# Performance work log

Measured on AMD Instinct MI355X. Metric: run time of the kernel, lower is better.

## Reference

```python
import jax, jax.numpy as jnp
import numpy as np

B, C_IN, H, W = 8, 128, 64, 64
C_KEY, C_VAL, C_OUT = 64, 64, 128
BN_EPS = 1e-5
NORM_EPS = 1e-7


def setup_inputs() -> dict:
    key = jax.random.key(0)
    ks = jax.random.split(key, 8)
    s = 0.02
    return {
        "query_feature": jax.random.normal(ks[0], (B, C_IN, H, W), jnp.float32),
        "key_feature": jax.random.normal(ks[1], (B, C_IN, H, W), jnp.float32),
        "value_feature": jax.random.normal(ks[2], (B, C_IN, H, W), jnp.float32),
        "Wk": jax.random.normal(ks[3], (C_KEY, C_IN), jnp.float32) * s,  # shared f_key/f_query 1x1 conv
        "bk": jnp.zeros((C_KEY,), jnp.float32),
        "gamma": jnp.ones((C_KEY,), jnp.float32),   # BatchNorm2d weight
        "beta": jnp.zeros((C_KEY,), jnp.float32),   # BatchNorm2d bias
        "Wv": jax.random.normal(ks[4], (C_VAL, C_IN), jnp.float32) * s,
        "bv": jnp.zeros((C_VAL,), jnp.float32),
        "Ww": jax.random.normal(ks[5], (C_OUT, C_VAL), jnp.float32) * s,  # zero-init in original; random for nontrivial output
        "bw": jnp.zeros((C_OUT,), jnp.float32),
    }


def _conv1x1(x, w, b):
    # x: [B,C,H,W], w: [O,C] -> [B,O,H,W]
    return jnp.einsum('bchw,oc->bohw', x, w) + b[None, :, None, None]


def _bn_train(y, gamma, beta):
    # BatchNorm2d in train mode: batch stats over (B,H,W) per channel
    m = y.mean(axis=(0, 2, 3), keepdims=True)
    v = y.var(axis=(0, 2, 3), keepdims=True)
    return (y - m) * jax.lax.rsqrt(v + BN_EPS) * gamma[None, :, None, None] + beta[None, :, None, None]


def reference(query_feature, key_feature, value_feature, Wk, bk, gamma, beta, Wv, bv, Ww, bw):
    b, _, h, w = query_feature.shape
    n = h * w

    def f_key(x):
        return _bn_train(_conv1x1(x, Wk, bk), gamma, beta)

    # query: [B,N,Ck], key: [B,Ck,N], value: [B,N,Cv]
    q = f_key(query_feature).reshape(b, C_KEY, n).transpose(0, 2, 1)
    k = f_key(key_feature).reshape(b, C_KEY, n)
    v = _conv1x1(value_feature, Wv, bv).reshape(b, C_VAL, n).transpose(0, 2, 1)

    # L2-normalize over channel dim (cosine similarity)
    q = q / (jnp.linalg.norm(q, axis=2, keepdims=True) + NORM_EPS)
    k = k / (jnp.linalg.norm(k, axis=1, keepdims=True) + NORM_EPS)

    sim = jnp.einsum('bnc,bcm->bnm', q, k) + 1.0     # [B,N,N], no softmax
    ctx = jnp.einsum('bnm,bmv->bnv', sim, v)         # [B,N,Cv]
    ctx = ctx.transpose(0, 2, 1).reshape(b, C_VAL, h, w)
    return _conv1x1(ctx, Ww, bw)
```

## Files before the change

kernel.cpp:

```cpp
#include <hip/hip_runtime.h>
#include <math.h>

#define NTOT 4096
#define NBATCH 8
#define CIN 128
#define CK 64
#define CV 64
#define CO 128
#define BN_COUNT 32768.0f

#define OFF_YQ    0ul
#define OFF_YK    2097152ul
#define OFF_V     4194304ul
#define OFF_STATS 6291456ul
#define OFF_VSUM  6307840ul
#define OFF_MP    2097152ul
#define OFF_DP    2228224ul

__global__ __launch_bounds__(256) void gemm3_fused(
    const float* __restrict__ Xq, const float* __restrict__ Xk, const float* __restrict__ Xv,
    const float* __restrict__ Wk, const float* __restrict__ bk,
    const float* __restrict__ Wv, const float* __restrict__ bv,
    float* __restrict__ Yq, float* __restrict__ Yk, float* __restrict__ Vv,
    float* __restrict__ stats, float* __restrict__ vsum)
{
    const int chunk = blockIdx.x;
    const int b     = blockIdx.y;
    const int which = blockIdx.z;
    const float* X    = (which == 0) ? Xq : (which == 1) ? Xk : Xv;
    const float* W    = (which == 2) ? Wv : Wk;
    const float* bias = (which == 2) ? bv : bk;
    float* Y          = (which == 0) ? Yq : (which == 1) ? Yk : Vv;

    __shared__ float sX[CIN][128];

    const int t = threadIdx.x;
    const int lane = t & 63;
    const int wu = __builtin_amdgcn_readfirstlane(t >> 6);

    const int n0 = chunk * 128;
    const float* Xb = X + (size_t)b * (CIN * NTOT) + n0;

#pragma unroll
    for (int r = 0; r < 16; ++r) {
        int idx4 = t + r * 256;
        int c  = idx4 >> 5;
        int j4 = (idx4 & 31) << 2;
        float4 xv = *(const float4*)(Xb + (size_t)c * NTOT + j4);
        *(float4*)&sX[c][j4] = xv;
    }
    __syncthreads();

    const float* Wp = W + (size_t)wu * 16 * CIN;
    float a0[16], a1[16];
#pragma unroll
    for (int ki = 0; ki < 16; ++ki) { a0[ki] = 0.f; a1[ki] = 0.f; }

#pragma unroll 8
    for (int c = 0; c < CIN; ++c) {
        float x0 = sX[c][lane];
        float x1 = sX[c][lane + 64];
#pragma unroll
        for (int ki = 0; ki < 16; ++ki) {
            float w = Wp[ki * CIN + c];
            a0[ki] += x0 * w;
            a1[ki] += x1 * w;
        }
    }

    float* Yb = Y + (size_t)b * (CK * NTOT) + n0;
#pragma unroll
    for (int ki = 0; ki < 16; ++ki) {
        const int o = wu * 16 + ki;
        const float bo = bias[o];
        float y0 = a0[ki] + bo;
        float y1 = a1[ki] + bo;
        Yb[(size_t)o * NTOT + lane]      = y0;
        Yb[(size_t)o * NTOT + lane + 64] = y1;
        a0[ki] = y0 + y1;
        a1[ki] = y0 * y0 + y1 * y1;
    }

#pragma unroll
    for (int off = 32; off > 0; off >>= 1) {
#pragma unroll
        for (int ki = 0; ki < 16; ++ki) {
            a0[ki] += __shfl_down(a0[ki], off, 64);
            a1[ki] += __shfl_down(a1[ki], off, 64);
        }
    }
    if (lane == 0) {
        if (which < 2) {
            float* sb = stats + (size_t)(b * 2 + which) * 1024;
#pragma unroll
            for (int ki = 0; ki < 16; ++ki) {
                const int o = wu * 16 + ki;
                atomicAdd(&sb[o * 16],     a0[ki]);
                atomicAdd(&sb[o * 16 + 4], a1[ki]);
            }
        } else {
            float* vb = vsum + (size_t)b * 1024;
#pragma unroll
            for (int ki = 0; ki < 16; ++ki)
                atomicAdd(&vb[(wu * 16 + ki) * 16], a0[ki]);
        }
    }
}

__global__ __launch_bounds__(256) void kv_kernel(
    const float* __restrict__ Yk, const float* __restrict__ Vv,
    const float* __restrict__ stats, const float* __restrict__ gamma,
    const float* __restrict__ beta, float* __restrict__ KVp)
{
    const int chunk = blockIdx.x;
    const int b     = blockIdx.y;
    __shared__ float sk[64][68];
    __shared__ float sv[64][68];
    __shared__ float rn[64];
    __shared__ float sscl[64], sshf[64];

    const int t = threadIdx.x;
    if (t < 64) {
        float S = 0.f, SS = 0.f;
#pragma unroll
        for (int bb = 0; bb < 8; ++bb) {
            const float* sb = stats + (size_t)(bb * 2 + 1) * 1024 + t * 16;
            S  += sb[0];
            SS += sb[4];
        }
        float mean = S * (1.f / BN_COUNT);
        float var  = SS * (1.f / BN_COUNT) - mean * mean;
        float scl  = gamma[t] * rsqrtf(var + 1e-5f);
        sscl[t] = scl;
        sshf[t] = beta[t] - mean * scl;
    }
    __syncthreads();

    const int n0 = chunk * 64;
    const float* Ykb = Yk + (size_t)b * (CK * NTOT) + n0;
    const float* Vb  = Vv + (size_t)b * (CK * NTOT) + n0;

#pragma unroll
    for (int r = 0; r < 4; ++r) {
        int idx4 = t + r * 256;
        int c  = idx4 >> 4;
        int j4 = (idx4 & 15) << 2;
        float4 kf = *(const float4*)(Ykb + (size_t)c * NTOT + j4);
        float4 vf = *(const float4*)(Vb  + (size_t)c * NTOT + j4);
        float scl = sscl[c], sh = sshf[c];
        float4 ks = make_float4(kf.x * scl + sh, kf.y * scl + sh,
                                kf.z * scl + sh, kf.w * scl + sh);
        *(float4*)&sk[c][j4] = ks;
        *(float4*)&sv[c][j4] = vf;
    }
    __syncthreads();

    if (t < 64) {
        float ssum = 0.f;
#pragma unroll 8
        for (int c = 0; c < 64; ++c) { float x = sk[c][t]; ssum += x * x; }
        rn[t] = 1.f / (sqrtf(ssum) + 1e-7f);
    }
    __syncthreads();
#pragma unroll
    for (int r = 0; r < 16; ++r) {
        int idx = t + r * 256;
        sk[idx >> 6][idx & 63] *= rn[idx & 63];
    }
    __syncthreads();

    const int tc = t >> 4, tv = t & 15;
    float acc[4][4];
#pragma unroll
    for (int i = 0; i < 4; ++i)
#pragma unroll
        for (int k2 = 0; k2 < 4; ++k2) acc[i][k2] = 0.f;

#pragma unroll 2
    for (int jq = 0; jq < 16; ++jq) {
        float4 a4[4], b4[4];
#pragma unroll
        for (int i = 0; i < 4; ++i)  a4[i] = *(const float4*)&sk[tc * 4 + i][jq * 4];
#pragma unroll
        for (int k2 = 0; k2 < 4; ++k2) b4[k2] = *(const float4*)&sv[tv * 4 + k2][jq * 4];
#pragma unroll
        for (int i = 0; i < 4; ++i)
#pragma unroll
            for (int k2 = 0; k2 < 4; ++k2) {
                acc[i][k2] += a4[i].x * b4[k2].x + a4[i].y * b4[k2].y
                            + a4[i].z * b4[k2].z + a4[i].w * b4[k2].w;
            }
    }

    float* P = KVp + ((size_t)(b * 64 + chunk)) * 4096;
#pragma unroll
    for (int i = 0; i < 4; ++i) {
        float4 st = make_float4(acc[i][0], acc[i][1], acc[i][2], acc[i][3]);
        *(float4*)&P[(tc * 4 + i) * 64 + tv * 4] = st;
    }
}

__global__ __launch_bounds__(256) void m_kernel(
    const float* __restrict__ KVp, const float* __restrict__ vsum,
    const float* __restrict__ Ww, const float* __restrict__ bw,
    float* __restrict__ Mp, float* __restrict__ dp)
{
    const int half = blockIdx.x;
    const int b    = blockIdx.y;
    __shared__ float sKV[64][36];
    __shared__ float sWw[128][36];
    __shared__ float svs[32];
    const int t = threadIdx.x;

#pragma unroll
    for (int r = 0; r < 4; ++r) {
        int idx4 = t + r * 256;
        int o  = idx4 >> 3;
        int v4 = (idx4 & 7) << 2;
        *(float4*)&sWw[o][v4] = *(const float4*)(Ww + (size_t)o * 64 + half * 32 + v4);
    }
    if (t < 32) svs[t] = vsum[((size_t)b * 64 + half * 32 + t) * 16];

    const float* base = KVp + (size_t)b * 64 * 4096;
    const int c0  = t >> 3;
    const int vq0 = (t & 7) << 2;
    const size_t off0 = (size_t)c0 * 64 + half * 32 + vq0;
    const size_t off1 = (size_t)(c0 + 32) * 64 + half * 32 + vq0;
    float4 r0 = make_float4(0.f, 0.f, 0.f, 0.f);
    float4 r1 = make_float4(0.f, 0.f, 0.f, 0.f);
#pragma unroll 4
    for (int ch = 0; ch < 64; ++ch) {
        const float* pc = base + (size_t)ch * 4096;
        float4 x0 = *(const float4*)(pc + off0);
        float4 x1 = *(const float4*)(pc + off1);
        r0.x += x0.x; r0.y += x0.y; r0.z += x0.z; r0.w += x0.w;
        r1.x += x1.x; r1.y += x1.y; r1.z += x1.z; r1.w += x1.w;
    }
    *(float4*)&sKV[c0][vq0]      = r0;
    *(float4*)&sKV[c0 + 32][vq0] = r1;
    __syncthreads();

    const int c  = t & 63;
    const int og = (t >> 6) * 32;
    float kreg[32];
#pragma unroll
    for (int vq = 0; vq < 8; ++vq) {
        float4 kv4 = *(const float4*)&sKV[c][vq * 4];
        kreg[vq * 4 + 0] = kv4.x; kreg[vq * 4 + 1] = kv4.y;
        kreg[vq * 4 + 2] = kv4.z; kreg[vq * 4 + 3] = kv4.w;
    }
    float* Mpb = Mp + ((size_t)b * 2 + half) * 8192;
#pragma unroll
    for (int oi = 0; oi < 32; ++oi) {
        const int o = og + oi;
        float acc = 0.f;
#pragma unroll
        for (int vq = 0; vq < 8; ++vq) {
            float4 w4 = *(const float4*)&sWw[o][vq * 4];
            acc += kreg[vq * 4 + 0] * w4.x + kreg[vq * 4 + 1] * w4.y
                 + kreg[vq * 4 + 2] * w4.z + kreg[vq * 4 + 3] * w4.w;
        }
        Mpb[(size_t)c * CO + o] = acc;
    }

    if (t < 128) {
        float acc = (half == 0) ? bw[t] : 0.f;
#pragma unroll 8
        for (int v = 0; v < 32; ++v) acc += sWw[t][v] * svs[v];
        dp[((size_t)b * 2 + half) * 128 + t] = acc;
    }
}

__global__ __launch_bounds__(256) void out_kernel(
    const float* __restrict__ Yq, const float* __restrict__ stats,
    const float* __restrict__ gamma, const float* __restrict__ beta,
    const float* __restrict__ Mp, const float* __restrict__ dp,
    float* __restrict__ out)
{
    const int chunk = blockIdx.x;
    const int b     = blockIdx.y;
    __shared__ float sM[CK * CO];
    __shared__ float sq[64][68];
    __shared__ float rn[64];
    __shared__ float sd[CO];
    __shared__ float sscl[64], sshf[64];

    const int t = threadIdx.x;
    const int n0 = chunk * 64;

    const float* Mp0 = Mp + (size_t)b * 2 * 8192;
    const float* Mp1 = Mp0 + 8192;
#pragma unroll
    for (int r = 0; r < 8; ++r) {
        int idx4 = t + r * 256;
        float4 m0 = ((const float4*)Mp0)[idx4];
        float4 m1 = ((const float4*)Mp1)[idx4];
        ((float4*)sM)[idx4] = make_float4(m0.x + m1.x, m0.y + m1.y,
                                          m0.z + m1.z, m0.w + m1.w);
    }
    if (t < CO) sd[t] = dp[(size_t)b * 2 * 128 + t] + dp[((size_t)b * 2 + 1) * 128 + t];
    if (t < 64) {
        float S = 0.f, SS = 0.f;
#pragma unroll
        for (int bb = 0; bb < 8; ++bb) {
            const float* sb = stats + (size_t)(bb * 2) * 1024 + t * 16;
            S  += sb[0];
            SS += sb[4];
        }
        float mean = S * (1.f / BN_COUNT);
        float var  = SS * (1.f / BN_COUNT) - mean * mean;
        float scl  = gamma[t] * rsqrtf(var + 1e-5f);
        sscl[t] = scl;
        sshf[t] = beta[t] - mean * scl;
    }
    __syncthreads();

    const float* Yb = Yq + (size_t)b * (CK * NTOT) + n0;
#pragma unroll
    for (int r = 0; r < 4; ++r) {
        int idx4 = t + r * 256;
        int c  = idx4 >> 4;
        int j4 = (idx4 & 15) << 2;
        float4 xv = *(const float4*)(Yb + (size_t)c * NTOT + j4);
        float scl = sscl[c], sh = sshf[c];
        sq[c][j4 + 0] = xv.x * scl + sh;
        sq[c][j4 + 1] = xv.y * scl + sh;
        sq[c][j4 + 2] = xv.z * scl + sh;
        sq[c][j4 + 3] = xv.w * scl + sh;
    }
    __syncthreads();
    if (t < 64) {
        float ssum = 0.f;
#pragma unroll 8
        for (int c = 0; c < 64; ++c) { float x = sq[c][t]; ssum += x * x; }
        rn[t] = 1.f / (sqrtf(ssum) + 1e-7f);
    }
    __syncthreads();

    const int j0 = (t & 15) << 2;
    const int o0 = (t >> 4) << 3;
    float acc[4][8];
#pragma unroll
    for (int jj = 0; jj < 4; ++jj)
#pragma unroll
        for (int oo = 0; oo < 8; ++oo) acc[jj][oo] = 0.f;

#pragma unroll 4
    for (int c = 0; c < 64; ++c) {
        float4 qv = *(const float4*)&sq[c][j0];
        float4 m0 = *(const float4*)&sM[c * CO + o0];
        float4 m1 = *(const float4*)&sM[c * CO + o0 + 4];
        float aq[4] = {qv.x, qv.y, qv.z, qv.w};
        float am[8] = {m0.x, m0.y, m0.z, m0.w, m1.x, m1.y, m1.z, m1.w};
#pragma unroll
        for (int jj = 0; jj < 4; ++jj)
#pragma unroll
            for (int oo = 0; oo < 8; ++oo) acc[jj][oo] += aq[jj] * am[oo];
    }

    float4 rq = *(const float4*)&rn[j0];
    float rnj[4] = {rq.x, rq.y, rq.z, rq.w};

    float* outb = out + (size_t)b * (CO * NTOT) + n0;
#pragma unroll
    for (int oo = 0; oo < 8; ++oo) {
        float dd = sd[o0 + oo];
        float4 st = make_float4(acc[0][oo] * rnj[0] + dd,
                                acc[1][oo] * rnj[1] + dd,
                                acc[2][oo] * rnj[2] + dd,
                                acc[3][oo] * rnj[3] + dd);
        *(float4*)&outb[(size_t)(o0 + oo) * NTOT + j0] = st;
    }
}

extern "C" void kernel_launch(void* const* d_in, const int* in_sizes, int n_in,
                              void* d_out, int out_size, void* d_ws, size_t ws_size,
                              hipStream_t stream) {
    (void)in_sizes; (void)n_in; (void)out_size; (void)ws_size;
    const float* q     = (const float*)d_in[0];
    const float* k     = (const float*)d_in[1];
    const float* v     = (const float*)d_in[2];
    const float* Wk    = (const float*)d_in[3];
    const float* bk    = (const float*)d_in[4];
    const float* gamma = (const float*)d_in[5];
    const float* beta  = (const float*)d_in[6];
    const float* Wv    = (const float*)d_in[7];
    const float* bv    = (const float*)d_in[8];
    const float* Ww    = (const float*)d_in[9];
    const float* bw    = (const float*)d_in[10];
    float* out = (float*)d_out;
    float* ws  = (float*)d_ws;

    float* Yq    = ws + OFF_YQ;
    float* Yk    = ws + OFF_YK;
    float* Vv    = ws + OFF_V;
    float* stats = ws + OFF_STATS;
    float* vsum  = ws + OFF_VSUM;
    float* Mp    = ws + OFF_MP;
    float* dp    = ws + OFF_DP;
    float* KVp   = out;

    hipMemsetAsync(stats, 0, (16384 + 8192) * sizeof(float), stream);

    gemm3_fused<<<dim3(32, NBATCH, 3), 256, 0, stream>>>(
        q, k, v, Wk, bk, Wv, bv, Yq, Yk, Vv, stats, vsum);
    kv_kernel<<<dim3(64, NBATCH), 256, 0, stream>>>(Yk, Vv, stats, gamma, beta, KVp);
    m_kernel<<<dim3(2, NBATCH), 256, 0, stream>>>(KVp, vsum, Ww, bw, Mp, dp);
    out_kernel<<<dim3(64, NBATCH), 256, 0, stream>>>(Yq, stats, gamma, beta, Mp, dp, out);
}
```

Baseline: 203.3 us.

## Split BN statistics into separate kernel and shrink projection GEMM tiles

The projection GEMM now computes 64 columns per block instead of 128, which doubles the grid to 1536 blocks and removes the in-kernel shuffle reductions and atomics for BN statistics. A new stats_kernel re-reads Yq and Yk to accumulate per-channel sums into a single global slot, and the value-sum reduction moves into kv_kernel. The L2-norm computation in kv and out kernels is spread across all four waves, and kv folds the normalization into the operand loads. The cost is an extra launch and an extra full read of Yq and Yk (about 16 MB).

```diff
diff --git a/kernel.cpp b/kernel.cpp
--- a/kernel.cpp
+++ b/kernel.cpp
@@ -13,16 +13,15 @@
 #define OFF_YK    2097152ul
 #define OFF_V     4194304ul
 #define OFF_STATS 6291456ul
-#define OFF_VSUM  6307840ul
+#define OFF_VSUM  6293504ul
 #define OFF_MP    2097152ul
 #define OFF_DP    2228224ul
 
-__global__ __launch_bounds__(256) void gemm3_fused(
+__global__ __launch_bounds__(256) void gemm3_kernel(
     const float* __restrict__ Xq, const float* __restrict__ Xk, const float* __restrict__ Xv,
     const float* __restrict__ Wk, const float* __restrict__ bk,
     const float* __restrict__ Wv, const float* __restrict__ bv,
-    float* __restrict__ Yq, float* __restrict__ Yk, float* __restrict__ Vv,
-    float* __restrict__ stats, float* __restrict__ vsum)
+    float* __restrict__ Yq, float* __restrict__ Yk, float* __restrict__ Vv)
 {
     const int chunk = blockIdx.x;
     const int b     = blockIdx.y;
@@ -32,102 +31,103 @@
     const float* bias = (which == 2) ? bv : bk;
     float* Y          = (which == 0) ? Yq : (which == 1) ? Yk : Vv;
 
-    __shared__ float sX[CIN][128];
+    __shared__ float sX[CIN][64];
 
     const int t = threadIdx.x;
     const int lane = t & 63;
     const int wu = __builtin_amdgcn_readfirstlane(t >> 6);
 
-    const int n0 = chunk * 128;
+    const int n0 = chunk * 64;
     const float* Xb = X + (size_t)b * (CIN * NTOT) + n0;
 
 #pragma unroll
-    for (int r = 0; r < 16; ++r) {
+    for (int r = 0; r < 8; ++r) {
         int idx4 = t + r * 256;
-        int c  = idx4 >> 5;
-        int j4 = (idx4 & 31) << 2;
+        int c  = idx4 >> 4;
+        int j4 = (idx4 & 15) << 2;
         float4 xv = *(const float4*)(Xb + (size_t)c * NTOT + j4);
         *(float4*)&sX[c][j4] = xv;
     }
     __syncthreads();
 
     const float* Wp = W + (size_t)wu * 16 * CIN;
-    float a0[16], a1[16];
-#pragma unroll
-    for (int ki = 0; ki < 16; ++ki) { a0[ki] = 0.f; a1[ki] = 0.f; }
+    float acc[16];
+#pragma unroll
+    for (int ki = 0; ki < 16; ++ki) acc[ki] = 0.f;
 
 #pragma unroll 8
     for (int c = 0; c < CIN; ++c) {
-        float x0 = sX[c][lane];
-        float x1 = sX[c][lane + 64];
-#pragma unroll
-        for (int ki = 0; ki < 16; ++ki) {
-            float w = Wp[ki * CIN + c];
-            a0[ki] += x0 * w;
-            a1[ki] += x1 * w;
-        }
+        float xv = sX[c][lane];
+#pragma unroll
+        for (int ki = 0; ki < 16; ++ki)
+            acc[ki] += xv * Wp[ki * CIN + c];
     }
 
     float* Yb = Y + (size_t)b * (CK * NTOT) + n0;
 #pragma unroll
     for (int ki = 0; ki < 16; ++ki) {
-        const int o = wu * 16 + ki;
-        const float bo = bias[o];
-        float y0 = a0[ki] + bo;
-        float y1 = a1[ki] + bo;
-        Yb[(size_t)o * NTOT + lane]      = y0;
-        Yb[(size_t)o * NTOT + lane + 64] = y1;
-        a0[ki] = y0 + y1;
-        a1[ki] = y0 * y0 + y1 * y1;
-    }
-
+        int o = wu * 16 + ki;
+        Yb[(size_t)o * NTOT + lane] = acc[ki] + bias[o];
+    }
+}
+
+__global__ __launch_bounds__(256) void stats_kernel(
+    const float* __restrict__ Yq, const float* __restrict__ Yk,
+    float* __restrict__ stats)
+{
+    const int nsplit = blockIdx.x;
+    const int c      = blockIdx.y;
+    const int which  = blockIdx.z;
+    const float* Y = which ? Yk : Yq;
+    const int t = threadIdx.x;
+
+    float s = 0.f, ss = 0.f;
+#pragma unroll
+    for (int p = 0; p < 4; ++p) {
+        int b = (t >> 7) + p * 2;
+        int e = (t & 127) << 2;
+        const float* src = Y + (size_t)b * (CK * NTOT) + (size_t)c * NTOT
+                         + nsplit * 512 + e;
+        float4 v = *(const float4*)src;
+        s  += v.x + v.y + v.z + v.w;
+        ss += v.x * v.x + v.y * v.y + v.z * v.z + v.w * v.w;
+    }
 #pragma unroll
     for (int off = 32; off > 0; off >>= 1) {
-#pragma unroll
-        for (int ki = 0; ki < 16; ++ki) {
-            a0[ki] += __shfl_down(a0[ki], off, 64);
-            a1[ki] += __shfl_down(a1[ki], off, 64);
-        }
-    }
-    if (lane == 0) {
-        if (which < 2) {
-            float* sb = stats + (size_t)(b * 2 + which) * 1024;
-#pragma unroll
-            for (int ki = 0; ki < 16; ++ki) {
-                const int o = wu * 16 + ki;
-                atomicAdd(&sb[o * 16],     a0[ki]);
-                atomicAdd(&sb[o * 16 + 4], a1[ki]);
-            }
-        } else {
-            float* vb = vsum + (size_t)b * 1024;
-#pragma unroll
-            for (int ki = 0; ki < 16; ++ki)
-                atomicAdd(&vb[(wu * 16 + ki) * 16], a0[ki]);
-        }
+        s  += __shfl_down(s, off, 64);
+        ss += __shfl_down(ss, off, 64);
+    }
+    __shared__ float red[8];
+    int wave = t >> 6, lane = t & 63;
+    if (lane == 0) { red[wave * 2] = s; red[wave * 2 + 1] = ss; }
+    __syncthreads();
+    if (t == 0) {
+        float S  = red[0] + red[2] + red[4] + red[6];
+        float SS = red[1] + red[3] + red[5] + red[7];
+        atomicAdd(&stats[(which * 64 + c) * 16],     S);
+        atomicAdd(&stats[(which * 64 + c) * 16 + 4], SS);
     }
 }
 
 __global__ __launch_bounds__(256) void kv_kernel(
     const float* __restrict__ Yk, const float* __restrict__ Vv,
     const float* __restrict__ stats, const float* __restrict__ gamma,
-    const float* __restrict__ beta, float* __restrict__ KVp)
+    const float* __restrict__ beta, float* __restrict__ KVp,
+    float* __restrict__ vsum)
 {
     const int chunk = blockIdx.x;
     const int b     = blockIdx.y;
     __shared__ float sk[64][68];
     __shared__ float sv[64][68];
+    __shared__ float pn[4][64];
     __shared__ float rn[64];
     __shared__ float sscl[64], sshf[64];
 
     const int t = threadIdx.x;
+    const int wave = t >> 6, lane = t & 63;
     if (t < 64) {
-        float S = 0.f, SS = 0.f;
-#pragma unroll
-        for (int bb = 0; bb < 8; ++bb) {
-            const float* sb = stats + (size_t)(bb * 2 + 1) * 1024 + t * 16;
-            S  += sb[0];
-            SS += sb[4];
-        }
+        float S  = stats[(64 + t) * 16];
+        float SS = stats[(64 + t) * 16 + 4];
         float mean = S * (1.f / BN_COUNT);
         float var  = SS * (1.f / BN_COUNT) - mean * mean;
         float scl  = gamma[t] * rsqrtf(var + 1e-5f);
@@ -155,18 +155,24 @@
     }
     __syncthreads();
 
-    if (t < 64) {
-        float ssum = 0.f;
-#pragma unroll 8
-        for (int c = 0; c < 64; ++c) { float x = sk[c][t]; ssum += x * x; }
-        rn[t] = 1.f / (sqrtf(ssum) + 1e-7f);
-    }
-    __syncthreads();
-#pragma unroll
-    for (int r = 0; r < 16; ++r) {
-        int idx = t + r * 256;
-        sk[idx >> 6][idx & 63] *= rn[idx & 63];
-    }
+    {
+        float s = 0.f;
+#pragma unroll
+        for (int i = 0; i < 16; ++i) { float x = sk[wave * 16 + i][lane]; s += x * x; }
+        pn[wave][lane] = s;
+    }
+    {
+        const int v = t >> 2, q = t & 3;
+        float s = 0.f;
+#pragma unroll
+        for (int i = 0; i < 16; ++i) s += sv[v][q * 16 + i];
+        s += __shfl_down(s, 2, 64);
+        s += __shfl_down(s, 1, 64);
+        if (q == 0) atomicAdd(&vsum[((size_t)b * 64 + v) * 16], s);
+    }
+    __syncthreads();
+    if (t < 64)
+        rn[t] = 1.f / (sqrtf(pn[0][t] + pn[1][t] + pn[2][t] + pn[3][t]) + 1e-7f);
     __syncthreads();
 
     const int tc = t >> 4, tv = t & 15;
@@ -178,9 +184,13 @@
 
 #pragma unroll 2
     for (int jq = 0; jq < 16; ++jq) {
+        float4 rq = *(const float4*)&rn[jq * 4];
         float4 a4[4], b4[4];
 #pragma unroll
-        for (int i = 0; i < 4; ++i)  a4[i] = *(const float4*)&sk[tc * 4 + i][jq * 4];
+        for (int i = 0; i < 4; ++i) {
+            float4 k4 = *(const float4*)&sk[tc * 4 + i][jq * 4];
+            a4[i] = make_float4(k4.x * rq.x, k4.y * rq.y, k4.z * rq.z, k4.w * rq.w);
+        }
 #pragma unroll
         for (int k2 = 0; k2 < 4; ++k2) b4[k2] = *(const float4*)&sv[tv * 4 + k2][jq * 4];
 #pragma unroll
@@ -281,11 +291,13 @@
     const int b     = blockIdx.y;
     __shared__ float sM[CK * CO];
     __shared__ float sq[64][68];
+    __shared__ float pn[4][64];
     __shared__ float rn[64];
     __shared__ float sd[CO];
     __shared__ float sscl[64], sshf[64];
 
     const int t = threadIdx.x;
+    const int wave = t >> 6, lane = t & 63;
     const int n0 = chunk * 64;
 
     const float* Mp0 = Mp + (size_t)b * 2 * 8192;
@@ -300,13 +312,8 @@
     }
     if (t < CO) sd[t] = dp[(size_t)b * 2 * 128 + t] + dp[((size_t)b * 2 + 1) * 128 + t];
     if (t < 64) {
-        float S = 0.f, SS = 0.f;
-#pragma unroll
-        for (int bb = 0; bb < 8; ++bb) {
-            const float* sb = stats + (size_t)(bb * 2) * 1024 + t * 16;
-            S  += sb[0];
-            SS += sb[4];
-        }
+        float S  = stats[t * 16];
+        float SS = stats[t * 16 + 4];
         float mean = S * (1.f / BN_COUNT);
         float var  = SS * (1.f / BN_COUNT) - mean * mean;
         float scl  = gamma[t] * rsqrtf(var + 1e-5f);
@@ -329,12 +336,16 @@
         sq[c][j4 + 3] = xv.w * scl + sh;
     }
     __syncthreads();
-    if (t < 64) {
-        float ssum = 0.f;
-#pragma unroll 8
-        for (int c = 0; c < 64; ++c) { float x = sq[c][t]; ssum += x * x; }
-        rn[t] = 1.f / (sqrtf(ssum) + 1e-7f);
-    }
+
+    {
+        float s = 0.f;
+#pragma unroll
+        for (int i = 0; i < 16; ++i) { float x = sq[wave * 16 + i][lane]; s += x * x; }
+        pn[wave][lane] = s;
+    }
+    __syncthreads();
+    if (t < 64)
+        rn[t] = 1.f / (sqrtf(pn[0][t] + pn[1][t] + pn[2][t] + pn[3][t]) + 1e-7f);
     __syncthreads();
 
     const int j0 = (t & 15) << 2;
@@ -400,11 +411,12 @@
     float* dp    = ws + OFF_DP;
     float* KVp   = out;
 
-    hipMemsetAsync(stats, 0, (16384 + 8192) * sizeof(float), stream);
-
-    gemm3_fused<<<dim3(32, NBATCH, 3), 256, 0, stream>>>(
-        q, k, v, Wk, bk, Wv, bv, Yq, Yk, Vv, stats, vsum);
-    kv_kernel<<<dim3(64, NBATCH), 256, 0, stream>>>(Yk, Vv, stats, gamma, beta, KVp);
+    hipMemsetAsync(stats, 0, (2048 + 8192) * sizeof(float), stream);
+
+    gemm3_kernel<<<dim3(64, NBATCH, 3), 256, 0, stream>>>(
+        q, k, v, Wk, bk, Wv, bv, Yq, Yk, Vv);
+    stats_kernel<<<dim3(8, 64, 2), 256, 0, stream>>>(Yq, Yk, stats);
+    kv_kernel<<<dim3(64, NBATCH), 256, 0, stream>>>(Yk, Vv, stats, gamma, beta, KVp, vsum);
     m_kernel<<<dim3(2, NBATCH), 256, 0, stream>>>(KVp, vsum, Ww, bw, Mp, dp);
     out_kernel<<<dim3(64, NBATCH), 256, 0, stream>>>(Yq, stats, gamma, beta, Mp, dp, out);
 }
```

Result: faster. 189.3 us (-6.9%).
